# Performance work log

Hardware: AMD Instinct MI355X
Metric: run time of the kernel (lower is better)

## Reference

```python
import jax, jax.numpy as jnp
import numpy as np

N = 8192          # nodes
E = 262144        # edges (avg degree 32)
IN = 32           # output_seq_len * in_channels
HID = 16          # hidden_channels
HEADS = 8
OUT = 32          # output_seq_len * out_channels
SLOPE = 0.2       # GATv2 leaky_relu negative_slope
EPS = 1e-12       # F.normalize eps


def setup_inputs() -> dict:
    key = jax.random.key(0)
    ks = jax.random.split(key, 12)
    g = lambda k, shape, fan: (jax.random.normal(k, shape, jnp.float32) / np.float32(np.sqrt(fan)))
    x = jax.random.normal(ks[0], (N, IN), jnp.float32)
    edge_index = jax.random.randint(ks[1], (2, E), 0, N, dtype=jnp.int64)
    # conv1: in=IN -> HEADS x HID, concat
    W1l = g(ks[2], (IN, HEADS * HID), IN)
    b1l = jnp.zeros((HEADS * HID,), jnp.float32)
    W1r = g(ks[3], (IN, HEADS * HID), IN)
    b1r = jnp.zeros((HEADS * HID,), jnp.float32)
    att1 = g(ks[4], (HEADS, HID), HID)
    bias1 = jnp.zeros((HEADS * HID,), jnp.float32)
    W2l = g(ks[5], (HEADS * HID, OUT), HEADS * HID)
    b2l = jnp.zeros((OUT,), jnp.float32)
    W2r = g(ks[6], (HEADS * HID, OUT), HEADS * HID)
    b2r = jnp.zeros((OUT,), jnp.float32)
    att2 = g(ks[7], (1, OUT), OUT)
    bias2 = jnp.zeros((OUT,), jnp.float32)
    return {"x": x, "edge_index": edge_index,
            "W1l": W1l, "b1l": b1l, "W1r": W1r, "b1r": b1r, "att1": att1, "bias1": bias1,
            "W2l": W2l, "b2l": b2l, "W2r": W2r, "b2r": b2r, "att2": att2, "bias2": bias2}


def gatv2_conv(x, src, dst, Wl, bl, Wr, br, att, bias, heads, C, concat):
    """GATv2Conv (eval mode, self-loops already in src/dst). x: [N, F]."""
    n = x.shape[0]
    xl = (x @ Wl + bl).reshape(n, heads, C)  # source transform
    xr = (x @ Wr + br).reshape(n, heads, C)  # target transform
    h = jax.nn.leaky_relu(xl[src] + xr[dst], SLOPE)        # [Etot, H, C]
    e = jnp.einsum('ehc,hc->eh', h, att)                    # [Etot, H]
    m = jax.ops.segment_max(e, dst, num_segments=n)         # stable softmax per target
    p = jnp.exp(e - m[dst])
    s = jax.ops.segment_sum(p, dst, num_segments=n)
    alpha = p / (s[dst] + 1e-16)                            # [Etot, H]
    out = jax.ops.segment_sum(alpha[:, :, None] * xl[src], dst, num_segments=n)  # [n, H, C]
    out = out.reshape(n, heads * C) if concat else out.mean(axis=1)
    return out + bias


def reference(x, edge_index, W1l, b1l, W1r, b1r, att1, bias1, W2l, b2l, W2r, b2r, att2, bias2):
    n = x.shape[0]
    loops = jnp.arange(n, dtype=edge_index.dtype)
    src = jnp.concatenate([edge_index[0], loops])
    dst = jnp.concatenate([edge_index[1], loops])
    h1 = gatv2_conv(x, src, dst, W1l, b1l, W1r, b1r, att1, bias1, HEADS, HID, True)
    h2 = gatv2_conv(h1, src, dst, W2l, b2l, W2r, b2r, att2, bias2, 1, OUT, False)
    norm = jnp.sqrt(jnp.sum(h2 * h2, axis=1, keepdims=True))
    z = h2 / jnp.maximum(norm, EPS)                         # F.normalize(p=2, dim=1)
    A_pred = jax.nn.sigmoid(z @ z.T)                        # [N, N]
    return (A_pred, z)
```

## Files before the change

### kernel.cpp

```cpp
#include <hip/hip_runtime.h>
#include <hip/hip_bf16.h>
#include <cstdint>
#include <cstddef>

typedef float f32x4 __attribute__((ext_vector_type(4)));
typedef short short8 __attribute__((ext_vector_type(8)));

#define SLOT_SHIFT 7

__device__ __forceinline__ float lrelu(float v){ return v > 0.f ? v : 0.2f*v; }
__device__ __forceinline__ float bf2f(ushort u){ return __uint_as_float(((unsigned)u) << 16); }

__global__ __launch_bounds__(128) void k_linear1(const float* __restrict__ x,
                          const float* __restrict__ W1l, const float* __restrict__ b1l,
                          const float* __restrict__ W1r, const float* __restrict__ b1r,
                          __hip_bfloat16* __restrict__ xl1b, float* __restrict__ xr1,
                          int* __restrict__ cur, int N){
  __shared__ float xs[16][32];
  int t = threadIdx.x;
  int gid = blockIdx.x*128 + t;
  if (gid < N) cur[gid] = gid << SLOT_SHIFT;
  int r0 = blockIdx.x * 16;
  float wl[32], wr[32];
  #pragma unroll
  for (int k = 0; k < 32; k++){ wl[k] = W1l[k*128 + t]; wr[k] = W1r[k*128 + t]; }
  float bl = b1l[t], br = b1r[t];
  #pragma unroll
  for (int i = 0; i < 4; i++){
    int idx = t + i*128;
    xs[idx >> 5][idx & 31] = x[r0*32 + idx];
  }
  __syncthreads();
  #pragma unroll 4
  for (int r = 0; r < 16; r++){
    float al = bl, ar = br;
    const float4* xv4 = (const float4*)xs[r];
    #pragma unroll
    for (int q = 0; q < 8; q++){
      float4 xv = xv4[q];
      al += xv.x*wl[q*4+0] + xv.y*wl[q*4+1] + xv.z*wl[q*4+2] + xv.w*wl[q*4+3];
      ar += xv.x*wr[q*4+0] + xv.y*wr[q*4+1] + xv.z*wr[q*4+2] + xv.w*wr[q*4+3];
    }
    xl1b[(size_t)(r0+r)*128 + t] = __float2bfloat16(al);
    xr1[(size_t)(r0+r)*128 + t] = ar;
  }
}

__global__ void k_scatter(const int* __restrict__ ei, int E, int N,
                          int* __restrict__ cur, int* __restrict__ ssrc){
  int i = blockIdx.x*blockDim.x + threadIdx.x;
  int tot = E + N;
  if (i >= tot) return;
  int s = (i < E) ? ei[i]     : (i - E);
  int d = (i < E) ? ei[E + i] : (i - E);
  int pos = atomicAdd(&cur[d], 1);
  ssrc[pos] = s;
}

__global__ __launch_bounds__(256) void k_conv1l2(const int* __restrict__ cur,
                       const int* __restrict__ ssrc,
                       const __hip_bfloat16* __restrict__ xl1b, const float* __restrict__ xr1,
                       const float* __restrict__ att1, const float* __restrict__ bias1,
                       const float* __restrict__ W2l, const float* __restrict__ b2l,
                       const float* __restrict__ W2r, const float* __restrict__ b2r,
                       __hip_bfloat16* __restrict__ xl2b, float* __restrict__ xr2){
  __shared__ float w2[8192];
  __shared__ float h1s[8][128];
  int t = threadIdx.x;
  for (int i = t; i < 4096; i += 256){ w2[i] = W2l[i]; w2[4096+i] = W2r[i]; }
  int sub = t >> 7;
  int f = t & 127;
  float at_f = att1[f];
  float b1f = bias1[f];
  const ushort* xb = (const ushort*)xl1b;
  int d0 = blockIdx.x*8;
  #pragma unroll
  for (int it = 0; it < 4; it++){
    int d = d0 + it*2 + sub;
    int j0 = d << SLOT_SHIFT, j1 = cur[d];
    float xr_f = xr1[(size_t)d*128 + f];
    float s0 = 0.f, a0 = 0.f, s1 = 0.f, a1 = 0.f;
    float s2 = 0.f, a2 = 0.f, s3 = 0.f, a3 = 0.f;
    int j = j0;
    for (; j + 3 < j1; j += 4){
      int4 s4 = *(const int4*)&ssrc[j];
      float xA = bf2f(xb[(size_t)s4.x*128 + f]);
      float xB = bf2f(xb[(size_t)s4.y*128 + f]);
      float xC = bf2f(xb[(size_t)s4.z*128 + f]);
      float xD = bf2f(xb[(size_t)s4.w*128 + f]);
      float tA = lrelu(xA + xr_f) * at_f;
      float tB = lrelu(xB + xr_f) * at_f;
      float tC = lrelu(xC + xr_f) * at_f;
      float tD = lrelu(xD + xr_f) * at_f;
      #pragma unroll
      for (int k = 1; k < 16; k <<= 1){
        tA += __shfl_xor(tA, k, 64);
        tB += __shfl_xor(tB, k, 64);
        tC += __shfl_xor(tC, k, 64);
        tD += __shfl_xor(tD, k, 64);
      }
      float p0 = __expf(tA), p1 = __expf(tB);
      float p2 = __expf(tC), p3 = __expf(tD);
      s0 += p0; a0 += p0*xA;
      s1 += p1; a1 += p1*xB;
      s2 += p2; a2 += p2*xC;
      s3 += p3; a3 += p3*xD;
    }
    for (; j < j1; j++){
      int src = ssrc[j];
      float xv = bf2f(xb[(size_t)src*128 + f]);
      float tv = lrelu(xv + xr_f) * at_f;
      #pragma unroll
      for (int k = 1; k < 16; k <<= 1) tv += __shfl_xor(tv, k, 64);
      float p = __expf(tv);
      s0 += p; a0 += p*xv;
    }
    float s = (s0 + s1) + (s2 + s3);
    float acc = (a0 + a1) + (a2 + a3);
    h1s[it*2 + sub][f] = acc/(s + 1e-16f) + b1f;
  }
  __syncthreads();
  #pragma unroll
  for (int k = 0; k < 2; k++){
    int oo = t + k*256;
    int r = oo >> 6;
    int idx = oo & 63;
    int c = idx & 31; bool left = idx < 32;
    const float* W = left ? w2 : w2 + 4096;
    float a = left ? b2l[c] : b2r[c];
    #pragma unroll 8
    for (int kk = 0; kk < 128; kk++) a += h1s[r][kk] * W[kk*32 + c];
    int d = d0 + r;
    if (left) xl2b[(size_t)d*32 + c] = __float2bfloat16(a);
    else      xr2[(size_t)d*32 + c] = a;
  }
}

__global__ __launch_bounds__(256) void k_conv2(const int* __restrict__ cur,
                       const int* __restrict__ ssrc,
                       const __hip_bfloat16* __restrict__ xl2b, const float* __restrict__ xr2,
                       const float* __restrict__ att2, const float* __restrict__ bias2,
                       float* __restrict__ z, __hip_bfloat16* __restrict__ zb){
  int t = threadIdx.x;
  int w = t >> 6, lane = t & 63;
  int half = lane >> 5, c = lane & 31;
  int d = blockIdx.x*4 + w;
  int j0 = d << SLOT_SHIFT, j1 = cur[d];
  float xr_c = xr2[(size_t)d*32 + c];
  float at_c = att2[c];
  const ushort* xb = (const ushort*)xl2b;
  float s0 = 0.f, a0 = 0.f, s1 = 0.f, a1 = 0.f;
  int j = j0 + half;
  for (; j + 2 < j1; j += 4){
    int srcA = ssrc[j], srcB = ssrc[j+2];
    float xA = bf2f(xb[(size_t)srcA*32 + c]);
    float xB = bf2f(xb[(size_t)srcB*32 + c]);
    float tA = lrelu(xA + xr_c) * at_c;
    float tB = lrelu(xB + xr_c) * at_c;
    #pragma unroll
    for (int k = 1; k < 32; k <<= 1){
      tA += __shfl_xor(tA, k, 64);
      tB += __shfl_xor(tB, k, 64);
    }
    float p0 = __expf(tA), p1 = __expf(tB);
    s0 += p0; a0 += p0*xA;
    s1 += p1; a1 += p1*xB;
  }
  for (; j < j1; j += 2){
    int src = ssrc[j];
    float xv = bf2f(xb[(size_t)src*32 + c]);
    float tv = lrelu(xv + xr_c) * at_c;
    #pragma unroll
    for (int k = 1; k < 32; k <<= 1) tv += __shfl_xor(tv, k, 64);
    float p = __expf(tv);
    s0 += p; a0 += p*xv;
  }
  float s = s0 + s1;
  float acc = a0 + a1;
  s   += __shfl_xor(s, 32, 64);
  acc += __shfl_xor(acc, 32, 64);
  float v = acc/(s + 1e-16f) + bias2[c];
  float ss = v*v;
  #pragma unroll
  for (int k = 1; k < 32; k <<= 1) ss += __shfl_xor(ss, k, 64);
  if (half == 0){
    float zv = v / fmaxf(sqrtf(ss), 1e-12f);
    z[(size_t)d*32 + c] = zv;
    zb[(size_t)d*32 + c] = __float2bfloat16(zv);
  }
}

__global__ __launch_bounds__(256) void k_adj(const __hip_bfloat16* __restrict__ zb,
                                             float* __restrict__ out, int N){
  __shared__ float tile[64][68];
  int tid = threadIdx.x;
  int w = tid >> 6, l = tid & 63;
  int hi = l >> 4, lo = l & 15;
  int r0 = blockIdx.y*64, c0 = blockIdx.x*64;
  short8 a = *(const short8*)(zb + (size_t)(r0 + w*16 + lo)*32 + hi*8);
  f32x4 acc[4];
  #pragma unroll
  for (int ct = 0; ct < 4; ct++){
    short8 b = *(const short8*)(zb + (size_t)(c0 + ct*16 + lo)*32 + hi*8);
    acc[ct] = __builtin_amdgcn_mfma_f32_16x16x32_bf16(a, b, (f32x4){0.f,0.f,0.f,0.f}, 0, 0, 0);
  }
  #pragma unroll
  for (int ct = 0; ct < 4; ct++){
    #pragma unroll
    for (int r = 0; r < 4; r++)
      tile[w*16 + hi*4 + r][ct*16 + lo] = 1.f/(1.f + __expf(-acc[ct][r]));
  }
  __syncthreads();
  #pragma unroll
  for (int k = 0; k < 4; k++){
    int g = tid + k*256;
    int row = g >> 4, c4 = (g & 15)*4;
    f32x4 v = *(const f32x4*)&tile[row][c4];
    *(f32x4*)&out[(size_t)(r0 + row)*N + c0 + c4] = v;
  }
}

extern "C" void kernel_launch(void* const* d_in, const int* in_sizes, int n_in,
                              void* d_out, int out_size, void* d_ws, size_t ws_size,
                              hipStream_t stream){
  const float* x     = (const float*)d_in[0];
  const int*   ei    = (const int*)  d_in[1];
  const float* W1l   = (const float*)d_in[2];
  const float* b1l   = (const float*)d_in[3];
  const float* W1r   = (const float*)d_in[4];
  const float* b1r   = (const float*)d_in[5];
  const float* att1  = (const float*)d_in[6];
  const float* bias1 = (const float*)d_in[7];
  const float* W2l   = (const float*)d_in[8];
  const float* b2l   = (const float*)d_in[9];
  const float* W2r   = (const float*)d_in[10];
  const float* b2r   = (const float*)d_in[11];
  const float* att2  = (const float*)d_in[12];
  const float* bias2 = (const float*)d_in[13];

  const int N = in_sizes[0] / 32;
  const int E = in_sizes[1] / 2;
  const int Etot = E + N;

  char* w = (char*)d_ws;
  size_t p = 0;
  auto take = [&](size_t bytes)->char*{
    char* r = w + p;
    p = (p + bytes + 255) & ~(size_t)255;
    return r;
  };
  int*   cur  = (int*)  take((size_t)N*4);
  int*   ssrc = (int*)  take(((size_t)N << SLOT_SHIFT)*4);
  __hip_bfloat16* xl1b = (__hip_bfloat16*)take((size_t)N*128*2);
  float* xr1  = (float*)take((size_t)N*128*4);
  __hip_bfloat16* xl2b = (__hip_bfloat16*)take((size_t)N*32*2);
  float* xr2  = (float*)take((size_t)N*32*4);
  __hip_bfloat16* zb = (__hip_bfloat16*)take((size_t)N*32*2);

  float* Apred = (float*)d_out;
  float* z     = Apred + (size_t)N*N;

  k_linear1<<<N/16, 128, 0, stream>>>(x, W1l, b1l, W1r, b1r, xl1b, xr1, cur, N);
  k_scatter<<<(Etot+255)/256, 256, 0, stream>>>(ei, E, N, cur, ssrc);
  k_conv1l2<<<N/8, 256, 0, stream>>>(cur, ssrc, xl1b, xr1, att1, bias1,
                                     W2l, b2l, W2r, b2r, xl2b, xr2);
  k_conv2  <<<N/4, 256, 0, stream>>>(cur, ssrc, xl2b, xr2, att2, bias2, z, zb);

  dim3 grid(N/64, N/64);
  k_adj    <<<grid, 256, 0, stream>>>(zb, Apred, N);
}
```

Measured before the change: 129.6 us.

## Compute GAT attention scores per edge-head in a separate pass without shuffles

Measured after the change: 125.1 us. -3.5%, faster.

```diff
diff --git a/kernel.cpp b/kernel.cpp
--- a/kernel.cpp
+++ b/kernel.cpp
@@ -8,8 +8,8 @@
 
 #define SLOT_SHIFT 7
 
-__device__ __forceinline__ float lrelu(float v){ return v > 0.f ? v : 0.2f*v; }
 __device__ __forceinline__ float bf2f(ushort u){ return __uint_as_float(((unsigned)u) << 16); }
+__device__ __forceinline__ float lrelu(float v){ return fmaxf(v, 0.2f*v); }
 
 __global__ __launch_bounds__(128) void k_linear1(const float* __restrict__ x,
                           const float* __restrict__ W1l, const float* __restrict__ b1l,
@@ -64,59 +64,76 @@
                        const float* __restrict__ W2l, const float* __restrict__ b2l,
                        const float* __restrict__ W2r, const float* __restrict__ b2r,
                        __hip_bfloat16* __restrict__ xl2b, float* __restrict__ xr2){
-  __shared__ float w2[8192];
+  __shared__ float p_s[2][128][8];
   __shared__ float h1s[8][128];
   int t = threadIdx.x;
-  for (int i = t; i < 4096; i += 256){ w2[i] = W2l[i]; w2[4096+i] = W2r[i]; }
-  int sub = t >> 7;
-  int f = t & 127;
-  float at_f = att1[f];
+  int sub = t >> 7, f = t & 127;
+  int hp = f & 7;
+  const ushort* xb = (const ushort*)xl1b;
+  float4 attr0 = *(const float4*)(att1 + hp*16);
+  float4 attr1 = *(const float4*)(att1 + hp*16 + 4);
+  float4 attr2 = *(const float4*)(att1 + hp*16 + 8);
+  float4 attr3 = *(const float4*)(att1 + hp*16 + 12);
   float b1f = bias1[f];
-  const ushort* xb = (const ushort*)xl1b;
   int d0 = blockIdx.x*8;
   #pragma unroll
   for (int it = 0; it < 4; it++){
     int d = d0 + it*2 + sub;
-    int j0 = d << SLOT_SHIFT, j1 = cur[d];
-    float xr_f = xr1[(size_t)d*128 + f];
-    float s0 = 0.f, a0 = 0.f, s1 = 0.f, a1 = 0.f;
-    float s2 = 0.f, a2 = 0.f, s3 = 0.f, a3 = 0.f;
-    int j = j0;
-    for (; j + 3 < j1; j += 4){
-      int4 s4 = *(const int4*)&ssrc[j];
-      float xA = bf2f(xb[(size_t)s4.x*128 + f]);
-      float xB = bf2f(xb[(size_t)s4.y*128 + f]);
-      float xC = bf2f(xb[(size_t)s4.z*128 + f]);
-      float xD = bf2f(xb[(size_t)s4.w*128 + f]);
-      float tA = lrelu(xA + xr_f) * at_f;
-      float tB = lrelu(xB + xr_f) * at_f;
-      float tC = lrelu(xC + xr_f) * at_f;
-      float tD = lrelu(xD + xr_f) * at_f;
-      #pragma unroll
-      for (int k = 1; k < 16; k <<= 1){
-        tA += __shfl_xor(tA, k, 64);
-        tB += __shfl_xor(tB, k, 64);
-        tC += __shfl_xor(tC, k, 64);
-        tD += __shfl_xor(tD, k, 64);
-      }
-      float p0 = __expf(tA), p1 = __expf(tB);
-      float p2 = __expf(tC), p3 = __expf(tD);
-      s0 += p0; a0 += p0*xA;
-      s1 += p1; a1 += p1*xB;
-      s2 += p2; a2 += p2*xC;
-      s3 += p3; a3 += p3*xD;
-    }
-    for (; j < j1; j++){
-      int src = ssrc[j];
-      float xv = bf2f(xb[(size_t)src*128 + f]);
-      float tv = lrelu(xv + xr_f) * at_f;
-      #pragma unroll
-      for (int k = 1; k < 16; k <<= 1) tv += __shfl_xor(tv, k, 64);
-      float p = __expf(tv);
-      s0 += p; a0 += p*xv;
-    }
-    float s = (s0 + s1) + (s2 + s3);
-    float acc = (a0 + a1) + (a2 + a3);
+    int j0 = d << SLOT_SHIFT;
+    int deg = cur[d] - j0;
+    float4 xr0 = *(const float4*)(xr1 + (size_t)d*128 + hp*16);
+    float4 xr1v = *(const float4*)(xr1 + (size_t)d*128 + hp*16 + 4);
+    float4 xr2v = *(const float4*)(xr1 + (size_t)d*128 + hp*16 + 8);
+    float4 xr3v = *(const float4*)(xr1 + (size_t)d*128 + hp*16 + 12);
+    __syncthreads();
+    int npair = deg*8;
+    for (int pr = f; pr < npair; pr += 128){
+      int jj = pr >> 3;
+      int src = ssrc[j0 + jj];
+      const short8* vp = (const short8*)(xb + (size_t)src*128 + hp*16);
+      short8 v0 = vp[0], v1 = vp[1];
+      float e, tv = 0.f;
+      e = bf2f((ushort)v0[0]) + xr0.x;  tv += lrelu(e)*attr0.x;
+      e = bf2f((ushort)v0[1]) + xr0.y;  tv += lrelu(e)*attr0.y;
+      e = bf2f((ushort)v0[2]) + xr0.z;  tv += lrelu(e)*attr0.z;
+      e = bf2f((ushort)v0[3]) + xr0.w;  tv += lrelu(e)*attr0.w;
+      e = bf2f((ushort)v0[4]) + xr1v.x; tv += lrelu(e)*attr1.x;
+      e = bf2f((ushort)v0[5]) + xr1v.y; tv += lrelu(e)*attr1.y;
+      e = bf2f((ushort)v0[6]) + xr1v.z; tv += lrelu(e)*attr1.z;
+      e = bf2f((ushort)v0[7]) + xr1v.w; tv += lrelu(e)*attr1.w;
+      e = bf2f((ushort)v1[0]) + xr2v.x; tv += lrelu(e)*attr2.x;
+      e = bf2f((ushort)v1[1]) + xr2v.y; tv += lrelu(e)*attr2.y;
+      e = bf2f((ushort)v1[2]) + xr2v.z; tv += lrelu(e)*attr2.z;
+      e = bf2f((ushort)v1[3]) + xr2v.w; tv += lrelu(e)*attr2.w;
+      e = bf2f((ushort)v1[4]) + xr3v.x; tv += lrelu(e)*attr3.x;
+      e = bf2f((ushort)v1[5]) + xr3v.y; tv += lrelu(e)*attr3.y;
+      e = bf2f((ushort)v1[6]) + xr3v.z; tv += lrelu(e)*attr3.z;
+      e = bf2f((ushort)v1[7]) + xr3v.w; tv += lrelu(e)*attr3.w;
+      p_s[sub][jj][hp] = __expf(tv);
+    }
+    __syncthreads();
+    int h2 = f >> 4;
+    float s = 0.f, acc = 0.f;
+    int jj = 0;
+    for (; jj + 3 < deg; jj += 4){
+      int4 s4 = *(const int4*)&ssrc[j0 + jj];
+      float p0 = p_s[sub][jj+0][h2];
+      float p1 = p_s[sub][jj+1][h2];
+      float p2 = p_s[sub][jj+2][h2];
+      float p3 = p_s[sub][jj+3][h2];
+      float x0 = bf2f(xb[(size_t)s4.x*128 + f]);
+      float x1 = bf2f(xb[(size_t)s4.y*128 + f]);
+      float x2 = bf2f(xb[(size_t)s4.z*128 + f]);
+      float x3 = bf2f(xb[(size_t)s4.w*128 + f]);
+      s   += (p0 + p1) + (p2 + p3);
+      acc += p0*x0 + p1*x1 + p2*x2 + p3*x3;
+    }
+    for (; jj < deg; jj++){
+      int src = ssrc[j0 + jj];
+      float p = p_s[sub][jj][h2];
+      float x = bf2f(xb[(size_t)src*128 + f]);
+      s += p; acc += p*x;
+    }
     h1s[it*2 + sub][f] = acc/(s + 1e-16f) + b1f;
   }
   __syncthreads();
@@ -126,7 +143,7 @@
     int r = oo >> 6;
     int idx = oo & 63;
     int c = idx & 31; bool left = idx < 32;
-    const float* W = left ? w2 : w2 + 4096;
+    const float* W = left ? W2l : W2r;
     float a = left ? b2l[c] : b2r[c];
     #pragma unroll 8
     for (int kk = 0; kk < 128; kk++) a += h1s[r][kk] * W[kk*32 + c];
@@ -141,42 +158,51 @@
                        const __hip_bfloat16* __restrict__ xl2b, const float* __restrict__ xr2,
                        const float* __restrict__ att2, const float* __restrict__ bias2,
                        float* __restrict__ z, __hip_bfloat16* __restrict__ zb){
+  __shared__ float p_s[4][128];
+  __shared__ float xr_s[4][32];
+  __shared__ float att_s[32];
   int t = threadIdx.x;
   int w = t >> 6, lane = t & 63;
+  int d = blockIdx.x*4 + w;
+  int j0 = d << SLOT_SHIFT;
+  int deg = cur[d] - j0;
+  if (t < 32) att_s[t] = att2[t];
+  if (lane < 32) xr_s[w][lane] = xr2[(size_t)d*32 + lane];
+  __syncthreads();
+  const ushort* xb = (const ushort*)xl2b;
+  for (int jj = lane; jj < deg; jj += 64){
+    int src = ssrc[j0 + jj];
+    const short8* vp = (const short8*)(xb + (size_t)src*32);
+    short8 v0 = vp[0], v1 = vp[1], v2 = vp[2], v3 = vp[3];
+    float tv = 0.f;
+    #pragma unroll
+    for (int k = 0; k < 8; k++){
+      float e0 = bf2f((ushort)v0[k]) + xr_s[w][k];      tv += lrelu(e0)*att_s[k];
+      float e1 = bf2f((ushort)v1[k]) + xr_s[w][8+k];    tv += lrelu(e1)*att_s[8+k];
+      float e2 = bf2f((ushort)v2[k]) + xr_s[w][16+k];   tv += lrelu(e2)*att_s[16+k];
+      float e3 = bf2f((ushort)v3[k]) + xr_s[w][24+k];   tv += lrelu(e3)*att_s[24+k];
+    }
+    p_s[w][jj] = __expf(tv);
+  }
+  __syncthreads();
   int half = lane >> 5, c = lane & 31;
-  int d = blockIdx.x*4 + w;
-  int j0 = d << SLOT_SHIFT, j1 = cur[d];
-  float xr_c = xr2[(size_t)d*32 + c];
-  float at_c = att2[c];
-  const ushort* xb = (const ushort*)xl2b;
   float s0 = 0.f, a0 = 0.f, s1 = 0.f, a1 = 0.f;
-  int j = j0 + half;
-  for (; j + 2 < j1; j += 4){
-    int srcA = ssrc[j], srcB = ssrc[j+2];
+  int jj = half;
+  for (; jj + 2 < deg; jj += 4){
+    int srcA = ssrc[j0 + jj], srcB = ssrc[j0 + jj + 2];
+    float pA = p_s[w][jj], pB = p_s[w][jj+2];
     float xA = bf2f(xb[(size_t)srcA*32 + c]);
     float xB = bf2f(xb[(size_t)srcB*32 + c]);
-    float tA = lrelu(xA + xr_c) * at_c;
-    float tB = lrelu(xB + xr_c) * at_c;
-    #pragma unroll
-    for (int k = 1; k < 32; k <<= 1){
-      tA += __shfl_xor(tA, k, 64);
-      tB += __shfl_xor(tB, k, 64);
-    }
-    float p0 = __expf(tA), p1 = __expf(tB);
-    s0 += p0; a0 += p0*xA;
-    s1 += p1; a1 += p1*xB;
-  }
-  for (; j < j1; j += 2){
-    int src = ssrc[j];
-    float xv = bf2f(xb[(size_t)src*32 + c]);
-    float tv = lrelu(xv + xr_c) * at_c;
-    #pragma unroll
-    for (int k = 1; k < 32; k <<= 1) tv += __shfl_xor(tv, k, 64);
-    float p = __expf(tv);
-    s0 += p; a0 += p*xv;
-  }
-  float s = s0 + s1;
-  float acc = a0 + a1;
+    s0 += pA; a0 += pA*xA;
+    s1 += pB; a1 += pB*xB;
+  }
+  for (; jj < deg; jj += 2){
+    int src = ssrc[j0 + jj];
+    float p = p_s[w][jj];
+    float x = bf2f(xb[(size_t)src*32 + c]);
+    s0 += p; a0 += p*x;
+  }
+  float s = s0 + s1, acc = a0 + a1;
   s   += __shfl_xor(s, 32, 64);
   acc += __shfl_xor(acc, 32, 64);
   float v = acc/(s + 1e-16f) + bias2[c];
```
